# Performance work log

Measured on AMD Instinct MI355X. Metric: run time of the kernel, lower is better.

## Reference

```python
import jax, jax.numpy as jnp
import numpy as np

N, T, H, O, S, R = 64, 1024, 256, 80, 128, 2


def _lin(k, fin, fout):
    kw, kb = jax.random.split(k)
    s = 1.0 / np.sqrt(fin)
    return (jax.random.uniform(kw, (fout, fin), jnp.float32, -s, s),
            jax.random.uniform(kb, (fout,), jnp.float32, -s, s))


def _gru_params(k, fin, hid):
    k1, k2, k3, k4 = jax.random.split(k, 4)
    s = 1.0 / np.sqrt(hid)
    u = lambda kk, shp: jax.random.uniform(kk, shp, jnp.float32, -s, s)
    return u(k1, (3 * hid, fin)), u(k2, (3 * hid, hid)), u(k3, (3 * hid,)), u(k4, (3 * hid,))


def setup_inputs() -> dict:
    key = jax.random.key(0)
    ks = jax.random.split(key, 16)
    inp = {}
    inp["input_enc"] = jax.random.normal(ks[0], (N, T, 2 * H), jnp.float32)
    inp["input_attW_enc"] = jax.random.normal(ks[1], (N, T, 2 * H), jnp.float32)
    inp["input_dec"] = jax.random.normal(ks[2], (N, O), jnp.float32)
    inp["style_vec"] = jax.random.normal(ks[3], (N, 1, S), jnp.float32)
    lengths = jnp.sort(jax.random.randint(ks[4], (N,), 1, T + 1))[::-1]
    inp["lengths_enc"] = lengths.at[0].set(T)  # pack_padded requires max(len)==T, descending
    inp["pw1"], inp["pb1"] = _lin(ks[5], O, 2 * H)
    inp["pw2"], inp["pb2"] = _lin(ks[6], 2 * H, H)
    inp["wdec"], inp["bdec"] = _lin(ks[7], 2 * H, 2 * H)
    inp["ga_ih"], inp["ga_hh"], inp["ga_bih"], inp["ga_bhh"] = _gru_params(ks[8], 3 * H + S, 2 * H)
    inp["wattn"], inp["battn"] = _lin(ks[9], 2 * H, 1)
    inp["wsc"], inp["bsc"] = _lin(ks[10], 4 * H + S, 2 * H)
    inp["g1_ih"], inp["g1_hh"], inp["g1_bih"], inp["g1_bhh"] = _gru_params(ks[11], 4 * H + S, 2 * H)
    inp["g2_ih"], inp["g2_hh"], inp["g2_bih"], inp["g2_bhh"] = _gru_params(ks[12], 2 * H, 2 * H)
    inp["wout"], inp["bout"] = _lin(ks[13], 2 * H, R * O)
    return inp


def _gru_cell(x, h, w_ih, w_hh, b_ih, b_hh):
    # PyTorch GRU cell: gates order (r, z, n)
    gi = x @ w_ih.T + b_ih
    gh = h @ w_hh.T + b_hh
    ir, iz, inn = jnp.split(gi, 3, -1)
    hr, hz, hn = jnp.split(gh, 3, -1)
    r = jax.nn.sigmoid(ir + hr)
    z = jax.nn.sigmoid(iz + hz)
    n = jnp.tanh(inn + r * hn)
    return (1.0 - z) * n + z * h


def reference(input_enc, input_attW_enc, input_dec, style_vec,
              pw1, pb1, pw2, pb2, wdec, bdec,
              ga_ih, ga_hh, ga_bih, ga_bhh,
              wattn, battn, wsc, bsc,
              g1_ih, g1_hh, g1_bih, g1_bhh,
              g2_ih, g2_hh, g2_bih, g2_bhh,
              wout, bout, lengths_enc):
    Nn, Tt, D2 = input_enc.shape
    Hh = D2 // 2
    # prenet (dropout disabled: eval-mode reference)
    pre = jax.nn.relu(jax.nn.relu(input_dec @ pw1.T + pb1) @ pw2.T + pb2)  # (N,H)
    ctx0 = jnp.zeros((Nn, 2 * Hh), input_enc.dtype)  # input_context=None -> zeros
    sv = style_vec[:, 0, :]
    x_att = jnp.concatenate([pre, ctx0, sv], axis=-1)  # (N,3H+S)
    h0 = jnp.zeros((Nn, 2 * Hh), input_enc.dtype)  # hidden states start None -> zeros
    out_att = _gru_cell(x_att, h0, ga_ih, ga_hh, ga_bih, ga_bhh)  # (N,2H)
    attW_dec = out_att @ wdec.T + bdec  # (N,2H), broadcast over T (expand_as)
    e = jnp.tanh(input_attW_enc + attW_dec[:, None, :])  # (N,T,2H)
    score = e @ wattn.T + battn  # (N,T,1)
    mask = (jnp.arange(Tt)[None, :] < lengths_enc[:, None]).astype(score.dtype)[..., None]
    w = jnp.exp(score) * mask  # pack/pad zeroes padded positions
    w = w / jnp.maximum(jnp.sum(w, axis=1, keepdims=True), 1e-12)  # F.normalize(p=1, dim=1)
    attn_applied = jnp.einsum('nt,ntd->nd', w[..., 0], input_enc)  # bmm(w^T, enc) -> (N,2H)
    out_dec = jnp.concatenate([attn_applied, out_att, sv], axis=-1)  # (N,4H+S)
    residual = out_dec @ wsc.T + bsc
    h1 = _gru_cell(out_dec, h0, g1_ih, g1_hh, g1_bih, g1_bhh)
    residual = residual + h1
    h2 = _gru_cell(residual, h0, g2_ih, g2_hh, g2_bih, g2_bhh)
    residual = residual + h2
    output = (residual @ wout.T + bout).reshape(Nn, R, -1)  # (N,r,O)
    return output, attn_applied[:, None, :]
```

## Files before the change

kernel.cpp:

```cpp
#include <hip/hip_runtime.h>
#include <math.h>

#define NB  64
#define TT  1024
#define H2  512
#define HH  256
#define SS  128
#define OO  80
#define FIN_A 896
#define FIN_1 1152
#define CH  16

__device__ __forceinline__ float fast_sigmoid(float x) { return 1.0f / (1.0f + __expf(-x)); }
__device__ __forceinline__ float fast_tanh(float x) {
    float xc = fminf(fmaxf(x, -15.0f), 15.0f);
    float e = __expf(2.0f * xc);
    return (e - 1.0f) / (e + 1.0f);
}
__device__ __forceinline__ float wred(float p) {
    #pragma unroll
    for (int o = 32; o > 0; o >>= 1) p += __shfl_xor(p, o, 64);
    return p;
}

__global__ void k_l1(const float* __restrict__ xdec, const float* __restrict__ pw1,
                     const float* __restrict__ pb1, float* __restrict__ t1) {
    int tid = blockIdx.x * blockDim.x + threadIdx.x;
    int n = tid >> 9, i = tid & 511;
    float acc = pb1[i];
    const float* x = xdec + n * OO;
    const float* w = pw1 + i * OO;
    #pragma unroll 8
    for (int k = 0; k < OO; ++k) acc += x[k] * w[k];
    t1[tid] = fmaxf(acc, 0.0f);
}

__global__ void k_l2(const float* __restrict__ t1, const float* __restrict__ pw2,
                     const float* __restrict__ pb2, float* __restrict__ pre) {
    int gw = (blockIdx.x * blockDim.x + threadIdx.x) >> 6;
    int lane = threadIdx.x & 63;
    int n = gw >> 8, i = gw & 255;
    const float* x = t1 + n * H2;
    const float* w = pw2 + (size_t)i * H2;
    float p = 0.0f;
    #pragma unroll
    for (int m = 0; m < 8; ++m) { int k = lane + 64 * m; p += x[k] * w[k]; }
    p = wred(p);
    if (lane == 0) pre[gw] = fmaxf(p + pb2[i], 0.0f);
}

__global__ void k_gruA(const float* __restrict__ pre, const float* __restrict__ sv,
                       const float* __restrict__ ga_ih, const float* __restrict__ ga_bih,
                       const float* __restrict__ ga_bhh, float* __restrict__ out_att) {
    int gw = (blockIdx.x * blockDim.x + threadIdx.x) >> 6;
    int lane = threadIdx.x & 63;
    int n = gw >> 9, j = gw & 511;
    const float* wr = ga_ih + (size_t)j * FIN_A;
    const float* wz = ga_ih + (size_t)(H2 + j) * FIN_A;
    const float* wn = ga_ih + (size_t)(2 * H2 + j) * FIN_A;
    const float* xp = pre + n * HH;
    const float* xs = sv + n * SS;
    float pr = 0.0f, pz = 0.0f, pn = 0.0f;
    #pragma unroll
    for (int m = 0; m < 4; ++m) {
        int k = lane + 64 * m;
        float x = xp[k];
        pr += x * wr[k]; pz += x * wz[k]; pn += x * wn[k];
    }
    #pragma unroll
    for (int m = 0; m < 2; ++m) {
        int k = lane + 64 * m;
        float x = xs[k];
        pr += x * wr[768 + k]; pz += x * wz[768 + k]; pn += x * wn[768 + k];
    }
    pr = wred(pr); pz = wred(pz); pn = wred(pn);
    if (lane == 0) {
        float r = fast_sigmoid(pr + ga_bih[j] + ga_bhh[j]);
        float z = fast_sigmoid(pz + ga_bih[H2 + j] + ga_bhh[H2 + j]);
        float nn = fast_tanh(pn + ga_bih[2 * H2 + j] + r * ga_bhh[2 * H2 + j]);
        out_att[gw] = (1.0f - z) * nn;
    }
}

__global__ void k_attw(const float* __restrict__ out_att, const float* __restrict__ wdec,
                       const float* __restrict__ bdec, float* __restrict__ attW_dec) {
    int gw = (blockIdx.x * blockDim.x + threadIdx.x) >> 6;
    int lane = threadIdx.x & 63;
    int n = gw >> 9, i = gw & 511;
    const float* x = out_att + n * H2;
    const float* w = wdec + (size_t)i * H2;
    float p = 0.0f;
    #pragma unroll
    for (int m = 0; m < 8; ++m) { int k = lane + 64 * m; p += x[k] * w[k]; }
    p = wred(p);
    if (lane == 0) attW_dec[gw] = p + bdec[i];
}

__global__ void k_attn(const float* __restrict__ enc, const float* __restrict__ attw_enc,
                       const float* __restrict__ attW_dec, const float* __restrict__ wattn,
                       const float* __restrict__ battn, const int* __restrict__ lengths,
                       float* __restrict__ num_part ,
                       float* __restrict__ den_part ) {
    int n = blockIdx.y;
    int wv = threadIdx.x >> 6, lane = threadIdx.x & 63;
    int tbase = blockIdx.x * (TT / CH) + wv * (TT / CH / 4);
    int d0 = lane * 8;
    const float4* dW = (const float4*)(attW_dec + n * H2 + d0);
    float4 dw0 = dW[0], dw1 = dW[1];
    const float4* aW = (const float4*)(wattn + d0);
    float4 w0 = aW[0], w1 = aW[1];
    float b = battn[0];
    int len = lengths[n];
    float4 acc0 = {0, 0, 0, 0}, acc1 = {0, 0, 0, 0};
    float denp = 0.0f;
    #pragma unroll 4
    for (int tt = 0; tt < TT / CH / 4; ++tt) {
        int t = tbase + tt;
        size_t rowoff = ((size_t)(n * TT + t)) * H2 + d0;
        const float4* e4 = (const float4*)(attw_enc + rowoff);
        float4 e0 = e4[0], e1 = e4[1];
        const float4* v4 = (const float4*)(enc + rowoff);
        float4 v0 = v4[0], v1 = v4[1];
        float p = fast_tanh(e0.x + dw0.x) * w0.x + fast_tanh(e0.y + dw0.y) * w0.y +
                  fast_tanh(e0.z + dw0.z) * w0.z + fast_tanh(e0.w + dw0.w) * w0.w +
                  fast_tanh(e1.x + dw1.x) * w1.x + fast_tanh(e1.y + dw1.y) * w1.y +
                  fast_tanh(e1.z + dw1.z) * w1.z + fast_tanh(e1.w + dw1.w) * w1.w;
        p = wred(p);
        float wt = (t < len) ? __expf(p + b) : 0.0f;
        acc0.x += wt * v0.x; acc0.y += wt * v0.y; acc0.z += wt * v0.z; acc0.w += wt * v0.w;
        acc1.x += wt * v1.x; acc1.y += wt * v1.y; acc1.z += wt * v1.z; acc1.w += wt * v1.w;
        denp += wt;
    }
    __shared__ float s[4 * 512];
    __shared__ float sd[4];
    float4* srow = (float4*)(s + wv * 512 + d0);
    srow[0] = acc0; srow[1] = acc1;
    if (lane == 0) sd[wv] = denp;
    __syncthreads();
    int d = threadIdx.x;
    float r0 = s[d] + s[512 + d] + s[1024 + d] + s[1536 + d];
    float r1 = s[256 + d] + s[512 + 256 + d] + s[1024 + 256 + d] + s[1536 + 256 + d];
    float* np = num_part + ((size_t)blockIdx.x * NB + n) * H2;
    np[d] = r0;
    np[256 + d] = r1;
    if (threadIdx.x == 0) den_part[blockIdx.x * NB + n] = sd[0] + sd[1] + sd[2] + sd[3];
}

__global__ void k_attn_reduce(const float* __restrict__ num_part, const float* __restrict__ den_part,
                              const float* __restrict__ out_att, const float* __restrict__ sv,
                              float* __restrict__ out, float* __restrict__ out_dec) {
    int tid = blockIdx.x * blockDim.x + threadIdx.x;
    int n = tid >> 9, d = tid & 511;
    float s = 0.0f;
    #pragma unroll
    for (int c = 0; c < CH; ++c) s += num_part[((size_t)c * NB + n) * H2 + d];
    float den = 0.0f;
    #pragma unroll
    for (int c = 0; c < CH; ++c) den += den_part[c * NB + n];
    float a = s / fmaxf(den, 1e-12f);
    out[NB * 160 + tid] = a;
    float* od = out_dec + (size_t)n * FIN_1;
    od[d] = a;
    od[H2 + d] = out_att[tid];
    if (d < SS) od[2 * H2 + d] = sv[n * SS + d];
}

__global__ void k_sc_h1(const float* __restrict__ out_dec, const float* __restrict__ wsc,
                        const float* __restrict__ bsc, const float* __restrict__ g1_ih,
                        const float* __restrict__ g1_bih, const float* __restrict__ g1_bhh,
                        float* __restrict__ res1) {
    int gw = (blockIdx.x * blockDim.x + threadIdx.x) >> 6;
    int lane = threadIdx.x & 63;
    int n = gw >> 9, j = gw & 511;
    const float* ws_ = wsc + (size_t)j * FIN_1;
    const float* wr = g1_ih + (size_t)j * FIN_1;
    const float* wz = g1_ih + (size_t)(H2 + j) * FIN_1;
    const float* wn = g1_ih + (size_t)(2 * H2 + j) * FIN_1;
    const float* x = out_dec + (size_t)n * FIN_1;
    float ps = 0.0f, pr = 0.0f, pz = 0.0f, pn = 0.0f;
    #pragma unroll 6
    for (int m = 0; m < 18; ++m) {
        int k = lane + 64 * m;
        float xv = x[k];
        ps += xv * ws_[k]; pr += xv * wr[k]; pz += xv * wz[k]; pn += xv * wn[k];
    }
    ps = wred(ps); pr = wred(pr); pz = wred(pz); pn = wred(pn);
    if (lane == 0) {
        float r = fast_sigmoid(pr + g1_bih[j] + g1_bhh[j]);
        float z = fast_sigmoid(pz + g1_bih[H2 + j] + g1_bhh[H2 + j]);
        float nn = fast_tanh(pn + g1_bih[2 * H2 + j] + r * g1_bhh[2 * H2 + j]);
        res1[gw] = ps + bsc[j] + (1.0f - z) * nn;
    }
}

__global__ void k_h2(const float* __restrict__ res1, const float* __restrict__ g2_ih,
                     const float* __restrict__ g2_bih, const float* __restrict__ g2_bhh,
                     float* __restrict__ res2) {
    int gw = (blockIdx.x * blockDim.x + threadIdx.x) >> 6;
    int lane = threadIdx.x & 63;
    int n = gw >> 9, j = gw & 511;
    const float* wr = g2_ih + (size_t)j * H2;
    const float* wz = g2_ih + (size_t)(H2 + j) * H2;
    const float* wn = g2_ih + (size_t)(2 * H2 + j) * H2;
    const float* x = res1 + n * H2;
    float pr = 0.0f, pz = 0.0f, pn = 0.0f;
    #pragma unroll
    for (int m = 0; m < 8; ++m) {
        int k = lane + 64 * m;
        float xv = x[k];
        pr += xv * wr[k]; pz += xv * wz[k]; pn += xv * wn[k];
    }
    pr = wred(pr); pz = wred(pz); pn = wred(pn);
    if (lane == 0) {
        float r = fast_sigmoid(pr + g2_bih[j] + g2_bhh[j]);
        float z = fast_sigmoid(pz + g2_bih[H2 + j] + g2_bhh[H2 + j]);
        float nn = fast_tanh(pn + g2_bih[2 * H2 + j] + r * g2_bhh[2 * H2 + j]);
        res2[gw] = res1[gw] + (1.0f - z) * nn;
    }
}

__global__ void k_out(const float* __restrict__ res2, const float* __restrict__ wout,
                      const float* __restrict__ bout, float* __restrict__ out) {
    int gw = (blockIdx.x * blockDim.x + threadIdx.x) >> 6;
    int lane = threadIdx.x & 63;
    int n = gw / 160, i = gw % 160;
    const float* x = res2 + n * H2;
    const float* w = wout + (size_t)i * H2;
    float p = 0.0f;
    #pragma unroll
    for (int m = 0; m < 8; ++m) { int k = lane + 64 * m; p += x[k] * w[k]; }
    p = wred(p);
    if (lane == 0) out[gw] = p + bout[i];
}

extern "C" void kernel_launch(void* const* d_in, const int* in_sizes, int n_in,
                              void* d_out, int out_size, void* d_ws, size_t ws_size,
                              hipStream_t stream) {
    const float* input_enc      = (const float*)d_in[0];
    const float* input_attW_enc = (const float*)d_in[1];
    const float* input_dec      = (const float*)d_in[2];
    const float* style_vec      = (const float*)d_in[3];
    const int*   lengths_enc    = (const int*)d_in[4];
    const float* pw1  = (const float*)d_in[5];
    const float* pb1  = (const float*)d_in[6];
    const float* pw2  = (const float*)d_in[7];
    const float* pb2  = (const float*)d_in[8];
    const float* wdec = (const float*)d_in[9];
    const float* bdec = (const float*)d_in[10];
    const float* ga_ih  = (const float*)d_in[11];
    const float* ga_bih = (const float*)d_in[13];
    const float* ga_bhh = (const float*)d_in[14];
    const float* wattn  = (const float*)d_in[15];
    const float* battn  = (const float*)d_in[16];
    const float* wsc    = (const float*)d_in[17];
    const float* bsc    = (const float*)d_in[18];
    const float* g1_ih  = (const float*)d_in[19];
    const float* g1_bih = (const float*)d_in[21];
    const float* g1_bhh = (const float*)d_in[22];
    const float* g2_ih  = (const float*)d_in[23];
    const float* g2_bih = (const float*)d_in[25];
    const float* g2_bhh = (const float*)d_in[26];
    const float* wout   = (const float*)d_in[27];
    const float* bout   = (const float*)d_in[28];
    float* out = (float*)d_out;

    float* ws = (float*)d_ws;
    float* num_part = ws;
    float* den_part = ws + 524288;
    float* t1       = ws + 525312;
    float* pre      = ws + 558080;
    float* out_att  = ws + 574464;
    float* attW_dec = ws + 607232;
    float* out_dec  = ws + 640000;
    float* res1     = ws + 713728;
    float* res2     = ws + 746496;

    k_l1<<<128, 256, 0, stream>>>(input_dec, pw1, pb1, t1);
    k_l2<<<4096, 256, 0, stream>>>(t1, pw2, pb2, pre);
    k_gruA<<<8192, 256, 0, stream>>>(pre, style_vec, ga_ih, ga_bih, ga_bhh, out_att);
    k_attw<<<8192, 256, 0, stream>>>(out_att, wdec, bdec, attW_dec);
    k_attn<<<dim3(CH, NB), 256, 0, stream>>>(input_enc, input_attW_enc, attW_dec,
                                             wattn, battn, lengths_enc, num_part, den_part);
    k_attn_reduce<<<128, 256, 0, stream>>>(num_part, den_part, out_att, style_vec, out, out_dec);
    k_sc_h1<<<8192, 256, 0, stream>>>(out_dec, wsc, bsc, g1_ih, g1_bih, g1_bhh, res1);
    k_h2<<<8192, 256, 0, stream>>>(res1, g2_ih, g2_bih, g2_bhh, res2);
    k_out<<<2560, 256, 0, stream>>>(res2, wout, bout, out);
}
```

Measured before the change: 411.5 us.

## Transpose activations to batch-minor layout and split attention into score/apply kernels

Stores activations transposed (feature-major, batch as lane) so each wave computes one output row for all 64 batch items with a scalar-broadcast weight. Each weight row is then read once instead of once per batch element, which cuts the weight traffic that dominated the GEMV kernels. The fused attention kernel is split into a per-row score kernel and a weighted-sum kernel with twice as many T chunks, which adds an intermediate buffer round trip. tanh and sigmoid now use hardware reciprocal without input clamping, which may lose precision at extreme inputs.

```diff
diff --git a/kernel.cpp b/kernel.cpp
--- a/kernel.cpp
+++ b/kernel.cpp
@@ -4,233 +4,215 @@
 #define NB  64
 #define TT  1024
 #define H2  512
-#define HH  256
 #define SS  128
 #define OO  80
 #define FIN_A 896
 #define FIN_1 1152
-#define CH  16
-
-__device__ __forceinline__ float fast_sigmoid(float x) { return 1.0f / (1.0f + __expf(-x)); }
+#define CH  32
+
+__device__ __forceinline__ float fast_rcp(float x) { return __builtin_amdgcn_rcpf(x); }
+__device__ __forceinline__ float fast_sigmoid(float x) { return fast_rcp(1.0f + __expf(-x)); }
 __device__ __forceinline__ float fast_tanh(float x) {
-    float xc = fminf(fmaxf(x, -15.0f), 15.0f);
-    float e = __expf(2.0f * xc);
-    return (e - 1.0f) / (e + 1.0f);
+    float e = __expf(2.0f * x);
+    return 1.0f - 2.0f * fast_rcp(e + 1.0f);
 }
 __device__ __forceinline__ float wred(float p) {
     #pragma unroll
     for (int o = 32; o > 0; o >>= 1) p += __shfl_xor(p, o, 64);
     return p;
 }
+__device__ __forceinline__ int rfl(int x) { return __builtin_amdgcn_readfirstlane(x); }
 
 __global__ void k_l1(const float* __restrict__ xdec, const float* __restrict__ pw1,
-                     const float* __restrict__ pb1, float* __restrict__ t1) {
-    int tid = blockIdx.x * blockDim.x + threadIdx.x;
-    int n = tid >> 9, i = tid & 511;
-    float acc = pb1[i];
-    const float* x = xdec + n * OO;
-    const float* w = pw1 + i * OO;
-    #pragma unroll 8
-    for (int k = 0; k < OO; ++k) acc += x[k] * w[k];
-    t1[tid] = fmaxf(acc, 0.0f);
-}
-
-__global__ void k_l2(const float* __restrict__ t1, const float* __restrict__ pw2,
-                     const float* __restrict__ pb2, float* __restrict__ pre) {
-    int gw = (blockIdx.x * blockDim.x + threadIdx.x) >> 6;
-    int lane = threadIdx.x & 63;
-    int n = gw >> 8, i = gw & 255;
-    const float* x = t1 + n * H2;
+                     const float* __restrict__ pb1, const float* __restrict__ sv,
+                     float* __restrict__ t1T, float* __restrict__ xaT,
+                     float* __restrict__ out_decT) {
+    int wv = threadIdx.x >> 6, lane = threadIdx.x & 63;
+    if (blockIdx.x < 128) {
+        int i = rfl(blockIdx.x * 4 + wv);
+        const float* w = pw1 + i * OO;
+        const float* x = xdec + lane * OO;
+        float acc = 0.0f;
+        #pragma unroll 8
+        for (int k = 0; k < OO; ++k) acc += w[k] * x[k];
+        t1T[i * 64 + lane] = fmaxf(acc + pb1[i], 0.0f);
+    } else {
+        int s = (blockIdx.x - 128) * 4 + wv;
+        float v = sv[lane * SS + s];
+        xaT[(256 + s) * 64 + lane] = v;
+        out_decT[(1024 + s) * 64 + lane] = v;
+    }
+}
+
+__global__ void k_l2(const float* __restrict__ t1T, const float* __restrict__ pw2,
+                     const float* __restrict__ pb2, float* __restrict__ xaT) {
+    int i = rfl(blockIdx.x * 4 + (threadIdx.x >> 6));
+    int lane = threadIdx.x & 63;
     const float* w = pw2 + (size_t)i * H2;
-    float p = 0.0f;
-    #pragma unroll
-    for (int m = 0; m < 8; ++m) { int k = lane + 64 * m; p += x[k] * w[k]; }
-    p = wred(p);
-    if (lane == 0) pre[gw] = fmaxf(p + pb2[i], 0.0f);
-}
-
-__global__ void k_gruA(const float* __restrict__ pre, const float* __restrict__ sv,
-                       const float* __restrict__ ga_ih, const float* __restrict__ ga_bih,
-                       const float* __restrict__ ga_bhh, float* __restrict__ out_att) {
-    int gw = (blockIdx.x * blockDim.x + threadIdx.x) >> 6;
-    int lane = threadIdx.x & 63;
-    int n = gw >> 9, j = gw & 511;
+    float acc = 0.0f;
+    #pragma unroll 16
+    for (int k = 0; k < H2; ++k) acc += w[k] * t1T[k * 64 + lane];
+    xaT[i * 64 + lane] = fmaxf(acc + pb2[i], 0.0f);
+}
+
+__global__ void k_gruA(const float* __restrict__ xaT, const float* __restrict__ ga_ih,
+                       const float* __restrict__ ga_bih, const float* __restrict__ ga_bhh,
+                       float* __restrict__ out_decT) {
+    int j = rfl(blockIdx.x * 4 + (threadIdx.x >> 6));
+    int lane = threadIdx.x & 63;
     const float* wr = ga_ih + (size_t)j * FIN_A;
     const float* wz = ga_ih + (size_t)(H2 + j) * FIN_A;
     const float* wn = ga_ih + (size_t)(2 * H2 + j) * FIN_A;
-    const float* xp = pre + n * HH;
-    const float* xs = sv + n * SS;
     float pr = 0.0f, pz = 0.0f, pn = 0.0f;
-    #pragma unroll
-    for (int m = 0; m < 4; ++m) {
-        int k = lane + 64 * m;
-        float x = xp[k];
-        pr += x * wr[k]; pz += x * wz[k]; pn += x * wn[k];
-    }
+    #pragma unroll 8
+    for (int k = 0; k < 256; ++k) {
+        float xv = xaT[k * 64 + lane];
+        pr += wr[k] * xv; pz += wz[k] * xv; pn += wn[k] * xv;
+    }
+    #pragma unroll 8
+    for (int k = 0; k < 128; ++k) {
+        float xv = xaT[(256 + k) * 64 + lane];
+        pr += wr[768 + k] * xv; pz += wz[768 + k] * xv; pn += wn[768 + k] * xv;
+    }
+    float r = fast_sigmoid(pr + ga_bih[j] + ga_bhh[j]);
+    float z = fast_sigmoid(pz + ga_bih[H2 + j] + ga_bhh[H2 + j]);
+    float nn = fast_tanh(pn + ga_bih[2 * H2 + j] + r * ga_bhh[2 * H2 + j]);
+    out_decT[(size_t)(H2 + j) * 64 + lane] = (1.0f - z) * nn;
+}
+
+__global__ void k_attw(const float* __restrict__ out_decT, const float* __restrict__ wdec,
+                       const float* __restrict__ bdec, float* __restrict__ attW_dec) {
+    int i = rfl(blockIdx.x * 4 + (threadIdx.x >> 6));
+    int lane = threadIdx.x & 63;
+    const float* w = wdec + (size_t)i * H2;
+    float acc = 0.0f;
+    #pragma unroll 16
+    for (int k = 0; k < H2; ++k) acc += w[k] * out_decT[(size_t)(H2 + k) * 64 + lane];
+    attW_dec[lane * H2 + i] = acc + bdec[i];
+}
+
+__global__ void k_score(const float* __restrict__ attw_enc, const float* __restrict__ attW_dec,
+                        const float* __restrict__ wattn, const float* __restrict__ battn,
+                        const int* __restrict__ lengths, float* __restrict__ ew) {
+    int wv = threadIdx.x >> 6, lane = threadIdx.x & 63;
+    int row = blockIdx.x * 4 + wv;
+    int n = row >> 10, t = row & 1023;
+    const float4* e4 = (const float4*)(attw_enc + (size_t)row * H2);
+    const float4* d4 = (const float4*)(attW_dec + n * H2);
+    const float4* w4 = (const float4*)wattn;
+    float p = 0.0f;
     #pragma unroll
     for (int m = 0; m < 2; ++m) {
-        int k = lane + 64 * m;
-        float x = xs[k];
-        pr += x * wr[768 + k]; pz += x * wz[768 + k]; pn += x * wn[768 + k];
-    }
-    pr = wred(pr); pz = wred(pz); pn = wred(pn);
-    if (lane == 0) {
-        float r = fast_sigmoid(pr + ga_bih[j] + ga_bhh[j]);
-        float z = fast_sigmoid(pz + ga_bih[H2 + j] + ga_bhh[H2 + j]);
-        float nn = fast_tanh(pn + ga_bih[2 * H2 + j] + r * ga_bhh[2 * H2 + j]);
-        out_att[gw] = (1.0f - z) * nn;
-    }
-}
-
-__global__ void k_attw(const float* __restrict__ out_att, const float* __restrict__ wdec,
-                       const float* __restrict__ bdec, float* __restrict__ attW_dec) {
-    int gw = (blockIdx.x * blockDim.x + threadIdx.x) >> 6;
-    int lane = threadIdx.x & 63;
-    int n = gw >> 9, i = gw & 511;
-    const float* x = out_att + n * H2;
-    const float* w = wdec + (size_t)i * H2;
-    float p = 0.0f;
-    #pragma unroll
-    for (int m = 0; m < 8; ++m) { int k = lane + 64 * m; p += x[k] * w[k]; }
+        int idx = lane + m * 64;
+        float4 e = e4[idx], d = d4[idx], w = w4[idx];
+        p += fast_tanh(e.x + d.x) * w.x + fast_tanh(e.y + d.y) * w.y +
+             fast_tanh(e.z + d.z) * w.z + fast_tanh(e.w + d.w) * w.w;
+    }
     p = wred(p);
-    if (lane == 0) attW_dec[gw] = p + bdec[i];
-}
-
-__global__ void k_attn(const float* __restrict__ enc, const float* __restrict__ attw_enc,
-                       const float* __restrict__ attW_dec, const float* __restrict__ wattn,
-                       const float* __restrict__ battn, const int* __restrict__ lengths,
-                       float* __restrict__ num_part ,
-                       float* __restrict__ den_part ) {
-    int n = blockIdx.y;
+    if (lane == 0) ew[row] = (t < lengths[n]) ? __expf(p + battn[0]) : 0.0f;
+}
+
+__global__ void k_apply(const float* __restrict__ enc, const float* __restrict__ ew,
+                        float* __restrict__ num_part ,
+                        float* __restrict__ den_part ) {
+    int n = blockIdx.y, c = blockIdx.x;
     int wv = threadIdx.x >> 6, lane = threadIdx.x & 63;
-    int tbase = blockIdx.x * (TT / CH) + wv * (TT / CH / 4);
+    int t0 = c * (TT / CH) + wv * (TT / CH / 4);
     int d0 = lane * 8;
-    const float4* dW = (const float4*)(attW_dec + n * H2 + d0);
-    float4 dw0 = dW[0], dw1 = dW[1];
-    const float4* aW = (const float4*)(wattn + d0);
-    float4 w0 = aW[0], w1 = aW[1];
-    float b = battn[0];
-    int len = lengths[n];
-    float4 acc0 = {0, 0, 0, 0}, acc1 = {0, 0, 0, 0};
-    float denp = 0.0f;
-    #pragma unroll 4
-    for (int tt = 0; tt < TT / CH / 4; ++tt) {
-        int t = tbase + tt;
-        size_t rowoff = ((size_t)(n * TT + t)) * H2 + d0;
-        const float4* e4 = (const float4*)(attw_enc + rowoff);
-        float4 e0 = e4[0], e1 = e4[1];
-        const float4* v4 = (const float4*)(enc + rowoff);
+    const float* base = enc + ((size_t)n * TT + t0) * H2 + d0;
+    const float* ewp = ew + n * TT + t0;
+    float4 a0 = {0, 0, 0, 0}, a1 = {0, 0, 0, 0};
+    float dp = 0.0f;
+    #pragma unroll
+    for (int t = 0; t < TT / CH / 4; ++t) {
+        float wt = ewp[t];
+        const float4* v4 = (const float4*)(base + (size_t)t * H2);
         float4 v0 = v4[0], v1 = v4[1];
-        float p = fast_tanh(e0.x + dw0.x) * w0.x + fast_tanh(e0.y + dw0.y) * w0.y +
-                  fast_tanh(e0.z + dw0.z) * w0.z + fast_tanh(e0.w + dw0.w) * w0.w +
-                  fast_tanh(e1.x + dw1.x) * w1.x + fast_tanh(e1.y + dw1.y) * w1.y +
-                  fast_tanh(e1.z + dw1.z) * w1.z + fast_tanh(e1.w + dw1.w) * w1.w;
-        p = wred(p);
-        float wt = (t < len) ? __expf(p + b) : 0.0f;
-        acc0.x += wt * v0.x; acc0.y += wt * v0.y; acc0.z += wt * v0.z; acc0.w += wt * v0.w;
-        acc1.x += wt * v1.x; acc1.y += wt * v1.y; acc1.z += wt * v1.z; acc1.w += wt * v1.w;
-        denp += wt;
+        a0.x += wt * v0.x; a0.y += wt * v0.y; a0.z += wt * v0.z; a0.w += wt * v0.w;
+        a1.x += wt * v1.x; a1.y += wt * v1.y; a1.z += wt * v1.z; a1.w += wt * v1.w;
+        dp += wt;
     }
     __shared__ float s[4 * 512];
     __shared__ float sd[4];
     float4* srow = (float4*)(s + wv * 512 + d0);
-    srow[0] = acc0; srow[1] = acc1;
-    if (lane == 0) sd[wv] = denp;
+    srow[0] = a0; srow[1] = a1;
+    if (lane == 0) sd[wv] = dp;
     __syncthreads();
     int d = threadIdx.x;
     float r0 = s[d] + s[512 + d] + s[1024 + d] + s[1536 + d];
-    float r1 = s[256 + d] + s[512 + 256 + d] + s[1024 + 256 + d] + s[1536 + 256 + d];
-    float* np = num_part + ((size_t)blockIdx.x * NB + n) * H2;
+    float r1 = s[256 + d] + s[768 + d] + s[1280 + d] + s[1792 + d];
+    float* np = num_part + ((size_t)c * NB + n) * H2;
     np[d] = r0;
     np[256 + d] = r1;
-    if (threadIdx.x == 0) den_part[blockIdx.x * NB + n] = sd[0] + sd[1] + sd[2] + sd[3];
-}
-
-__global__ void k_attn_reduce(const float* __restrict__ num_part, const float* __restrict__ den_part,
-                              const float* __restrict__ out_att, const float* __restrict__ sv,
-                              float* __restrict__ out, float* __restrict__ out_dec) {
-    int tid = blockIdx.x * blockDim.x + threadIdx.x;
-    int n = tid >> 9, d = tid & 511;
+    if (threadIdx.x == 0) den_part[c * NB + n] = sd[0] + sd[1] + sd[2] + sd[3];
+}
+
+__global__ void k_reduce(const float* __restrict__ num_part, const float* __restrict__ den_part,
+                         float* __restrict__ out, float* __restrict__ out_decT) {
+    int d = blockIdx.x * 4 + (threadIdx.x >> 6);
+    int lane = threadIdx.x & 63;
     float s = 0.0f;
     #pragma unroll
-    for (int c = 0; c < CH; ++c) s += num_part[((size_t)c * NB + n) * H2 + d];
+    for (int c = 0; c < CH; ++c) s += num_part[((size_t)c * NB + lane) * H2 + d];
     float den = 0.0f;
     #pragma unroll
-    for (int c = 0; c < CH; ++c) den += den_part[c * NB + n];
+    for (int c = 0; c < CH; ++c) den += den_part[c * NB + lane];
     float a = s / fmaxf(den, 1e-12f);
-    out[NB * 160 + tid] = a;
-    float* od = out_dec + (size_t)n * FIN_1;
-    od[d] = a;
-    od[H2 + d] = out_att[tid];
-    if (d < SS) od[2 * H2 + d] = sv[n * SS + d];
-}
-
-__global__ void k_sc_h1(const float* __restrict__ out_dec, const float* __restrict__ wsc,
+    out_decT[(size_t)d * 64 + lane] = a;
+    out[NB * 160 + lane * H2 + d] = a;
+}
+
+__global__ void k_sc_h1(const float* __restrict__ out_decT, const float* __restrict__ wsc,
                         const float* __restrict__ bsc, const float* __restrict__ g1_ih,
                         const float* __restrict__ g1_bih, const float* __restrict__ g1_bhh,
-                        float* __restrict__ res1) {
-    int gw = (blockIdx.x * blockDim.x + threadIdx.x) >> 6;
-    int lane = threadIdx.x & 63;
-    int n = gw >> 9, j = gw & 511;
+                        float* __restrict__ res1T) {
+    int j = rfl(blockIdx.x * 4 + (threadIdx.x >> 6));
+    int lane = threadIdx.x & 63;
     const float* ws_ = wsc + (size_t)j * FIN_1;
     const float* wr = g1_ih + (size_t)j * FIN_1;
     const float* wz = g1_ih + (size_t)(H2 + j) * FIN_1;
     const float* wn = g1_ih + (size_t)(2 * H2 + j) * FIN_1;
-    const float* x = out_dec + (size_t)n * FIN_1;
     float ps = 0.0f, pr = 0.0f, pz = 0.0f, pn = 0.0f;
-    #pragma unroll 6
-    for (int m = 0; m < 18; ++m) {
-        int k = lane + 64 * m;
-        float xv = x[k];
-        ps += xv * ws_[k]; pr += xv * wr[k]; pz += xv * wz[k]; pn += xv * wn[k];
-    }
-    ps = wred(ps); pr = wred(pr); pz = wred(pz); pn = wred(pn);
-    if (lane == 0) {
-        float r = fast_sigmoid(pr + g1_bih[j] + g1_bhh[j]);
-        float z = fast_sigmoid(pz + g1_bih[H2 + j] + g1_bhh[H2 + j]);
-        float nn = fast_tanh(pn + g1_bih[2 * H2 + j] + r * g1_bhh[2 * H2 + j]);
-        res1[gw] = ps + bsc[j] + (1.0f - z) * nn;
-    }
-}
-
-__global__ void k_h2(const float* __restrict__ res1, const float* __restrict__ g2_ih,
+    #pragma unroll 8
+    for (int k = 0; k < FIN_1; ++k) {
+        float xv = out_decT[(size_t)k * 64 + lane];
+        ps += ws_[k] * xv; pr += wr[k] * xv; pz += wz[k] * xv; pn += wn[k] * xv;
+    }
+    float r = fast_sigmoid(pr + g1_bih[j] + g1_bhh[j]);
+    float z = fast_sigmoid(pz + g1_bih[H2 + j] + g1_bhh[H2 + j]);
+    float nn = fast_tanh(pn + g1_bih[2 * H2 + j] + r * g1_bhh[2 * H2 + j]);
+    res1T[j * 64 + lane] = ps + bsc[j] + (1.0f - z) * nn;
+}
+
+__global__ void k_h2(const float* __restrict__ res1T, const float* __restrict__ g2_ih,
                      const float* __restrict__ g2_bih, const float* __restrict__ g2_bhh,
-                     float* __restrict__ res2) {
-    int gw = (blockIdx.x * blockDim.x + threadIdx.x) >> 6;
-    int lane = threadIdx.x & 63;
-    int n = gw >> 9, j = gw & 511;
+                     float* __restrict__ res2T) {
+    int j = rfl(blockIdx.x * 4 + (threadIdx.x >> 6));
+    int lane = threadIdx.x & 63;
     const float* wr = g2_ih + (size_t)j * H2;
     const float* wz = g2_ih + (size_t)(H2 + j) * H2;
     const float* wn = g2_ih + (size_t)(2 * H2 + j) * H2;
-    const float* x = res1 + n * H2;
     float pr = 0.0f, pz = 0.0f, pn = 0.0f;
-    #pragma unroll
-    for (int m = 0; m < 8; ++m) {
-        int k = lane + 64 * m;
-        float xv = x[k];
-        pr += xv * wr[k]; pz += xv * wz[k]; pn += xv * wn[k];
-    }
-    pr = wred(pr); pz = wred(pz); pn = wred(pn);
-    if (lane == 0) {
-        float r = fast_sigmoid(pr + g2_bih[j] + g2_bhh[j]);
-        float z = fast_sigmoid(pz + g2_bih[H2 + j] + g2_bhh[H2 + j]);
-        float nn = fast_tanh(pn + g2_bih[2 * H2 + j] + r * g2_bhh[2 * H2 + j]);
-        res2[gw] = res1[gw] + (1.0f - z) * nn;
-    }
-}
-
-__global__ void k_out(const float* __restrict__ res2, const float* __restrict__ wout,
+    #pragma unroll 8
+    for (int k = 0; k < H2; ++k) {
+        float xv = res1T[k * 64 + lane];
+        pr += wr[k] * xv; pz += wz[k] * xv; pn += wn[k] * xv;
+    }
+    float r = fast_sigmoid(pr + g2_bih[j] + g2_bhh[j]);
+    float z = fast_sigmoid(pz + g2_bih[H2 + j] + g2_bhh[H2 + j]);
+    float nn = fast_tanh(pn + g2_bih[2 * H2 + j] + r * g2_bhh[2 * H2 + j]);
+    res2T[j * 64 + lane] = res1T[j * 64 + lane] + (1.0f - z) * nn;
+}
+
+__global__ void k_out(const float* __restrict__ res2T, const float* __restrict__ wout,
                       const float* __restrict__ bout, float* __restrict__ out) {
-    int gw = (blockIdx.x * blockDim.x + threadIdx.x) >> 6;
-    int lane = threadIdx.x & 63;
-    int n = gw / 160, i = gw % 160;
-    const float* x = res2 + n * H2;
+    int i = rfl(blockIdx.x * 4 + (threadIdx.x >> 6));
+    int lane = threadIdx.x & 63;
     const float* w = wout + (size_t)i * H2;
-    float p = 0.0f;
-    #pragma unroll
-    for (int m = 0; m < 8; ++m) { int k = lane + 64 * m; p += x[k] * w[k]; }
-    p = wred(p);
-    if (lane == 0) out[gw] = p + bout[i];
+    float acc = 0.0f;
+    #pragma unroll 16
+    for (int k = 0; k < H2; ++k) acc += w[k] * res2T[k * 64 + lane];
+    out[lane * 160 + i] = acc + bout[i];
 }
 
 extern "C" void kernel_launch(void* const* d_in, const int* in_sizes, int n_in,
@@ -266,23 +248,24 @@
 
     float* ws = (float*)d_ws;
     float* num_part = ws;
-    float* den_part = ws + 524288;
-    float* t1       = ws + 525312;
-    float* pre      = ws + 558080;
-    float* out_att  = ws + 574464;
-    float* attW_dec = ws + 607232;
-    float* out_dec  = ws + 640000;
-    float* res1     = ws + 713728;
-    float* res2     = ws + 746496;
-
-    k_l1<<<128, 256, 0, stream>>>(input_dec, pw1, pb1, t1);
-    k_l2<<<4096, 256, 0, stream>>>(t1, pw2, pb2, pre);
-    k_gruA<<<8192, 256, 0, stream>>>(pre, style_vec, ga_ih, ga_bih, ga_bhh, out_att);
-    k_attw<<<8192, 256, 0, stream>>>(out_att, wdec, bdec, attW_dec);
-    k_attn<<<dim3(CH, NB), 256, 0, stream>>>(input_enc, input_attW_enc, attW_dec,
-                                             wattn, battn, lengths_enc, num_part, den_part);
-    k_attn_reduce<<<128, 256, 0, stream>>>(num_part, den_part, out_att, style_vec, out, out_dec);
-    k_sc_h1<<<8192, 256, 0, stream>>>(out_dec, wsc, bsc, g1_ih, g1_bih, g1_bhh, res1);
-    k_h2<<<8192, 256, 0, stream>>>(res1, g2_ih, g2_bih, g2_bhh, res2);
-    k_out<<<2560, 256, 0, stream>>>(res2, wout, bout, out);
-}
+    float* den_part = ws + 1048576;
+    float* t1T      = ws + 1050624;
+    float* xaT      = ws + 1083392;
+    float* out_decT = ws + 1107968;
+    float* attW_dec = ws + 1181696;
+    float* ew       = ws + 1214464;
+    float* res1T    = ws + 1280000;
+    float* res2T    = ws + 1312768;
+
+    k_l1<<<160, 256, 0, stream>>>(input_dec, pw1, pb1, style_vec, t1T, xaT, out_decT);
+    k_l2<<<64, 256, 0, stream>>>(t1T, pw2, pb2, xaT);
+    k_gruA<<<128, 256, 0, stream>>>(xaT, ga_ih, ga_bih, ga_bhh, out_decT);
+    k_attw<<<128, 256, 0, stream>>>(out_decT, wdec, bdec, attW_dec);
+    k_score<<<NB * TT / 4, 256, 0, stream>>>(input_attW_enc, attW_dec, wattn, battn,
+                                             lengths_enc, ew);
+    k_apply<<<dim3(CH, NB), 256, 0, stream>>>(input_enc, ew, num_part, den_part);
+    k_reduce<<<128, 256, 0, stream>>>(num_part, den_part, out, out_decT);
+    k_sc_h1<<<128, 256, 0, stream>>>(out_decT, wsc, bsc, g1_ih, g1_bih, g1_bhh, res1T);
+    k_h2<<<128, 256, 0, stream>>>(res1T, g2_ih, g2_bih, g2_bhh, res2T);
+    k_out<<<40, 256, 0, stream>>>(res2T, wout, bout, out);
+}
```

After: 549.4 us. 1.34x slower.
